# Performance work log

Measured on AMD Instinct MI355X. Metric: run time of the kernel, lower is better.

Reference implementation:

```python
import jax, jax.numpy as jnp
import numpy as np

D_IN = 384
HID = 384
D_OUT = 384

def _kaiming(key, fan_in, fan_out):
    return jax.random.normal(key, (fan_in, fan_out), dtype=jnp.float32) * np.sqrt(2.0 / fan_in)

def setup_inputs() -> dict:
    key = jax.random.key(0)
    ks = jax.random.split(key, 12)
    B, O, T = 8, 1024, 8192
    obj_vecs = jax.random.normal(ks[0], (B, O, D_IN), dtype=jnp.float32)
    pred_vecs = jax.random.normal(ks[1], (B, T, D_IN), dtype=jnp.float32)
    edges = jax.random.randint(ks[2], (B, T, 2), 0, O, dtype=jnp.int64)
    # gconv1: [3D -> H -> 2H + Dout]; gconv2: [H -> H -> Dout]
    w1a = _kaiming(ks[3], 3 * D_IN, HID); b1a = jnp.zeros((HID,), jnp.float32)
    w1b = _kaiming(ks[4], HID, 2 * HID + D_OUT); b1b = jnp.zeros((2 * HID + D_OUT,), jnp.float32)
    w2a = _kaiming(ks[5], HID, HID); b2a = jnp.zeros((HID,), jnp.float32)
    w2b = _kaiming(ks[6], HID, D_OUT); b2b = jnp.zeros((D_OUT,), jnp.float32)
    return {"obj_vecs": obj_vecs, "pred_vecs": pred_vecs, "edges": edges,
            "w1a": w1a, "b1a": b1a, "w1b": w1b, "b1b": b1b,
            "w2a": w2a, "b2a": b2a, "w2b": w2b, "b2b": b2b}

def _gconv_forward(obj_vecs, pred_vecs, edges, w1a, b1a, w1b, b1b, w2a, b2a, w2b, b2b):
    B, O, D = obj_vecs.shape
    s_idx = edges[:, :, 0]  # (B, T)
    o_idx = edges[:, :, 1]
    batch = jnp.arange(B)[:, None]
    subj = obj_vecs[batch, s_idx]  # (B, T, D) gather
    objt = obj_vecs[batch, o_idx]
    triple = jnp.concatenate([subj, pred_vecs, objt], axis=-1)  # (B, T, 3D)
    h = jax.nn.relu(triple @ w1a + b1a)
    t = jax.nn.relu(h @ w1b + b1b)  # (B, T, 2H + Dout)
    new_s = t[:, :, :HID]
    new_p = t[:, :, HID:HID + D_OUT]
    new_o = t[:, :, HID + D_OUT:]
    # scatter_add per batch into (O, H) buffers
    def agg(si, oi, vs, vo):
        return jnp.zeros((O, HID), vs.dtype).at[si].add(vs).at[oi].add(vo)
    pooled = jax.vmap(agg)(s_idx, o_idx, new_s, new_o)  # (B, O, H)
    pooled = pooled / jnp.linalg.norm(pooled)  # global Frobenius norm, as in torch .norm()
    out_obj = jax.nn.relu(jax.nn.relu(pooled @ w2a + b2a) @ w2b + b2b)
    return out_obj, new_p

def reference(obj_vecs, pred_vecs, edges, w1a, b1a, w1b, b1b, w2a, b2a, w2b, b2b):
    return _gconv_forward(obj_vecs, pred_vecs, edges, w1a, b1a, w1b, b1b, w2a, b2a, w2b, b2b)
```

## Files before the change

### kernel.cpp

```cpp
#include <hip/hip_runtime.h>
#include <hip/hip_bf16.h>

#define NB 8
#define NT 8192
#define NO 1024
#define DD 384
#define K1 1152
#define M1 65536
#define MO 8192

typedef __attribute__((ext_vector_type(8))) short bf16x8;
typedef __attribute__((ext_vector_type(4))) float f32x4;
typedef __attribute__((ext_vector_type(4))) unsigned short u16x4;

__device__ __forceinline__ unsigned short f2bf(float f) {
    union { float f; unsigned u; } v; v.f = f;
    unsigned r = v.u + 0x7FFFu + ((v.u >> 16) & 1u);
    return (unsigned short)(r >> 16);
}
__device__ __forceinline__ float bf2f(unsigned short h) {
    union { unsigned u; float f; } v; v.u = ((unsigned)h) << 16;
    return v.f;
}
__device__ __forceinline__ bf16x8 pack8(f32x4 a, f32x4 b) {
    bf16x8 r;
    r[0] = (short)f2bf(a[0]); r[1] = (short)f2bf(a[1]);
    r[2] = (short)f2bf(a[2]); r[3] = (short)f2bf(a[3]);
    r[4] = (short)f2bf(b[0]); r[5] = (short)f2bf(b[1]);
    r[6] = (short)f2bf(b[2]); r[7] = (short)f2bf(b[3]);
    return r;
}
__device__ __forceinline__ void gload16(const void* g, void* l) {
    __builtin_amdgcn_global_load_lds(
        (const __attribute__((address_space(1))) unsigned int*)g,
        (__attribute__((address_space(3))) unsigned int*)l, 16, 0, 0);
}

__global__ void k_cvt4(const float* __restrict__ s, unsigned short* __restrict__ d, int n) {
    int i = (blockIdx.x * blockDim.x + threadIdx.x) * 4;
    if (i >= n) return;
    f32x4 v = *(const f32x4*)(s + i);
    u16x4 o;
    o[0] = f2bf(v[0]); o[1] = f2bf(v[1]); o[2] = f2bf(v[2]); o[3] = f2bf(v[3]);
    *(u16x4*)(d + i) = o;
}
__global__ void k_tr(const float* __restrict__ s, unsigned short* __restrict__ d, int K, int N) {
    int k = blockIdx.x;
    int n = blockIdx.y * blockDim.x + threadIdx.x;
    if (n < N) d[n * K + k] = f2bf(s[k * N + n]);
}

__global__ void k_ss1(const float* __restrict__ p, float* __restrict__ partial, int n4) {
    __shared__ float wsum[4];
    int stride = gridDim.x * blockDim.x;
    float s = 0.f;
    for (int i = blockIdx.x * blockDim.x + threadIdx.x; i < n4; i += stride) {
        f32x4 v = *(const f32x4*)(p + i * 4);
        s += v[0] * v[0] + v[1] * v[1] + v[2] * v[2] + v[3] * v[3];
    }
#pragma unroll
    for (int off = 32; off; off >>= 1) s += __shfl_down(s, off, 64);
    if ((threadIdx.x & 63) == 0) wsum[threadIdx.x >> 6] = s;
    __syncthreads();
    if (threadIdx.x == 0)
        partial[blockIdx.x] = wsum[0] + wsum[1] + wsum[2] + wsum[3];
}
__global__ void k_ss2(const float* __restrict__ partial, float* __restrict__ o) {
    float s = partial[threadIdx.x];
#pragma unroll
    for (int off = 32; off; off >>= 1) s += __shfl_down(s, off, 64);
    __shared__ float w0, w1;
    if (threadIdx.x == 0) w0 = s;
    if (threadIdx.x == 64) w1 = s;
    __syncthreads();
    if (threadIdx.x == 0) o[0] = w0 + w1;
}
__global__ void k_normcvt(const float* __restrict__ p, const float* __restrict__ ss,
                          unsigned short* __restrict__ o) {
    int i = (blockIdx.x * blockDim.x + threadIdx.x) * 8;
    float s = rsqrtf(ss[0]);
    f32x4 a = *(const f32x4*)(p + i), b = *(const f32x4*)(p + i + 4);
    a *= s; b *= s;
    *(bf16x8*)(o + i) = pack8(a, b);
}

__global__ void k_hist(const int* __restrict__ edges, int* __restrict__ cnt) {
    int i = blockIdx.x * 256 + threadIdx.x;
    int2 e = *(const int2*)&edges[(size_t)i * 2];
    int b = i >> 13;
    atomicAdd(&cnt[(b << 10) + e.x], 1);
    atomicAdd(&cnt[(b << 10) + e.y], 1);
}
__global__ void k_scan(const int* __restrict__ cnt, int* __restrict__ offs) {
    __shared__ int a[1024];
    int b = blockIdx.x, t = threadIdx.x;
    int own = cnt[(b << 10) + t];
    a[t] = own;
    __syncthreads();
    for (int s = 1; s < 1024; s <<= 1) {
        int v = (t >= s) ? a[t - s] : 0;
        __syncthreads();
        a[t] += v;
        __syncthreads();
    }
    offs[(b << 10) + t] = a[t] - own;
}
__global__ void k_fill(const int* __restrict__ edges, const int* __restrict__ offs,
                       int* __restrict__ cur, int* __restrict__ elist) {
    int i = blockIdx.x * 256 + threadIdx.x;
    int2 e = *(const int2*)&edges[(size_t)i * 2];
    int b = i >> 13, t = i & (NT - 1);
    int ps = atomicAdd(&cur[(b << 10) + e.x], 1);
    elist[(b << 14) + offs[(b << 10) + e.x] + ps] = t * 2;
    int po = atomicAdd(&cur[(b << 10) + e.y], 1);
    elist[(b << 14) + offs[(b << 10) + e.y] + po] = t * 2 + 1;
}
__global__ void k_pool(const unsigned short* __restrict__ sob, const int* __restrict__ cnt,
                       const int* __restrict__ offs, const int* __restrict__ elist,
                       float* __restrict__ pooled) {
    int w = (blockIdx.x * 256 + threadIdx.x) >> 6;
    int lane = threadIdx.x & 63;
    if (lane >= 48) return;
    int b = w >> 10, o = w & (NO - 1);
    int len = cnt[(b << 10) + o];
    const int* lst = elist + (b << 14) + offs[(b << 10) + o];
    f32x4 a0 = {0.f, 0.f, 0.f, 0.f}, a1 = {0.f, 0.f, 0.f, 0.f};
    f32x4 c0 = {0.f, 0.f, 0.f, 0.f}, c1 = {0.f, 0.f, 0.f, 0.f};
    int j = 0;
    for (; j + 1 < len; j += 2) {
        int e0 = lst[j], e1 = lst[j + 1];
        bf16x8 v0 = *(const bf16x8*)(sob + ((size_t)((b << 13) + (e0 >> 1))) * 768 + (e0 & 1) * DD + lane * 8);
        bf16x8 v1 = *(const bf16x8*)(sob + ((size_t)((b << 13) + (e1 >> 1))) * 768 + (e1 & 1) * DD + lane * 8);
        a0[0] += bf2f((unsigned short)v0[0]); a0[1] += bf2f((unsigned short)v0[1]);
        a0[2] += bf2f((unsigned short)v0[2]); a0[3] += bf2f((unsigned short)v0[3]);
        a1[0] += bf2f((unsigned short)v0[4]); a1[1] += bf2f((unsigned short)v0[5]);
        a1[2] += bf2f((unsigned short)v0[6]); a1[3] += bf2f((unsigned short)v0[7]);
        c0[0] += bf2f((unsigned short)v1[0]); c0[1] += bf2f((unsigned short)v1[1]);
        c0[2] += bf2f((unsigned short)v1[2]); c0[3] += bf2f((unsigned short)v1[3]);
        c1[0] += bf2f((unsigned short)v1[4]); c1[1] += bf2f((unsigned short)v1[5]);
        c1[2] += bf2f((unsigned short)v1[6]); c1[3] += bf2f((unsigned short)v1[7]);
    }
    if (j < len) {
        int e0 = lst[j];
        bf16x8 v0 = *(const bf16x8*)(sob + ((size_t)((b << 13) + (e0 >> 1))) * 768 + (e0 & 1) * DD + lane * 8);
        a0[0] += bf2f((unsigned short)v0[0]); a0[1] += bf2f((unsigned short)v0[1]);
        a0[2] += bf2f((unsigned short)v0[2]); a0[3] += bf2f((unsigned short)v0[3]);
        a1[0] += bf2f((unsigned short)v0[4]); a1[1] += bf2f((unsigned short)v0[5]);
        a1[2] += bf2f((unsigned short)v0[6]); a1[3] += bf2f((unsigned short)v0[7]);
    }
    a0 += c0; a1 += c1;
    float* dst = pooled + ((size_t)((b << 10) + o)) * DD + lane * 8;
    *(f32x4*)dst = a0;
    *(f32x4*)(dst + 4) = a1;
}

__launch_bounds__(256, 2)
__global__ void gemm_g1(const unsigned short* __restrict__ objb,
                        const float* __restrict__ predf,
                        const int* __restrict__ edges,
                        const unsigned short* __restrict__ Bt,
                        const float* __restrict__ bias,
                        unsigned short* __restrict__ outb)
{
    const int tid = threadIdx.x;
    const int lane = tid & 63;
    const int d = blockIdx.x;
    const int chunk = gridDim.x >> 3;
    const int bid = (d & 7) * chunk + (d >> 3);
    const int xb = bid >> 1, nb = bid & 1;
    const int m0 = xb * 128;
    const int btrow = nb * 192;

    __shared__ unsigned short lds[2][20480];

    const int rb = tid >> 3;
    const int c8 = ((tid & 7) ^ (rb & 7)) * 8;

    const int bb = (m0 >> 13) << 10;
    int er0[4], er1[4];
#pragma unroll
    for (int i = 0; i < 4; ++i) {
        int2 e = *(const int2*)&edges[(size_t)(m0 + i * 32 + rb) * 2];
        er0[i] = bb + e.x;
        er1[i] = bb + e.y;
    }

    f32x4 acc[4][6];
#pragma unroll
    for (int i = 0; i < 4; ++i)
#pragma unroll
        for (int j = 0; j < 6; ++j) acc[i][j] = (f32x4){0.f, 0.f, 0.f, 0.f};

    const int wid = tid >> 6, wm = wid >> 1, wn = wid & 1;
    const int l16 = lane & 15, lg = lane >> 4;

#pragma unroll
    for (int i = 0; i < 4; ++i)
        gload16(objb + (size_t)er0[i] * DD + c8, &lds[0][i * 2048 + tid * 8]);
#pragma unroll
    for (int i = 0; i < 6; ++i)
        gload16(Bt + (size_t)(btrow + i * 32 + rb) * K1 + c8, &lds[0][8192 + i * 2048 + tid * 8]);

    const int nsteps = K1 / 64;
    for (int t = 0; t < nsteps; ++t) {
        const int cur = t & 1;
        const int tn = t + 1;
        if (tn < nsteps) {
            const int nseg = tn / 6;
            const int ko = (tn - nseg * 6) * 64;
            if (nseg == 1) {
                f32x4 pf[4][2];
#pragma unroll
                for (int i = 0; i < 4; ++i) {
                    const float* p = predf + (size_t)(m0 + i * 32 + rb) * DD + ko + c8;
                    pf[i][0] = *(const f32x4*)p;
                    pf[i][1] = *(const f32x4*)(p + 4);
                }
#pragma unroll
                for (int i = 0; i < 6; ++i)
                    gload16(Bt + (size_t)(btrow + i * 32 + rb) * K1 + tn * 64 + c8,
                            &lds[cur ^ 1][8192 + i * 2048 + tid * 8]);
#pragma unroll
                for (int i = 0; i < 4; ++i)
                    *(bf16x8*)(&lds[cur ^ 1][i * 2048 + tid * 8]) = pack8(pf[i][0], pf[i][1]);
            } else {
#pragma unroll
                for (int i = 0; i < 4; ++i) {
                    int row = (nseg == 0) ? er0[i] : er1[i];
                    gload16(objb + (size_t)row * DD + ko + c8, &lds[cur ^ 1][i * 2048 + tid * 8]);
                }
#pragma unroll
                for (int i = 0; i < 6; ++i)
                    gload16(Bt + (size_t)(btrow + i * 32 + rb) * K1 + tn * 64 + c8,
                            &lds[cur ^ 1][8192 + i * 2048 + tid * 8]);
                asm volatile("s_waitcnt vmcnt(10)" ::: "memory");
            }
        } else {
            asm volatile("s_waitcnt vmcnt(0)" ::: "memory");
        }
        __builtin_amdgcn_s_barrier();
        const unsigned short* At = &lds[cur][0];
        const unsigned short* Bl = &lds[cur][8192];
#pragma unroll
        for (int kt = 0; kt < 2; ++kt) {
            const int cs = ((kt * 4 + lg) ^ (l16 & 7)) * 8;
            bf16x8 af[4], bfr[6];
#pragma unroll
            for (int mt = 0; mt < 4; ++mt)
                af[mt] = *(const bf16x8*)(At + (wm * 64 + mt * 16 + l16) * 64 + cs);
#pragma unroll
            for (int nn = 0; nn < 6; ++nn)
                bfr[nn] = *(const bf16x8*)(Bl + (wn * 96 + nn * 16 + l16) * 64 + cs);
#pragma unroll
            for (int mt = 0; mt < 4; ++mt)
#pragma unroll
                for (int nn = 0; nn < 6; ++nn)
                    acc[mt][nn] = __builtin_amdgcn_mfma_f32_16x16x32_bf16(af[mt], bfr[nn], acc[mt][nn], 0, 0, 0);
        }
        asm volatile("s_waitcnt lgkmcnt(0)" ::: "memory");
        __builtin_amdgcn_s_barrier();
    }

#pragma unroll
    for (int nn = 0; nn < 6; ++nn) {
        int gn = btrow + wn * 96 + nn * 16 + l16;
        float bv = bias[gn];
#pragma unroll
        for (int mt = 0; mt < 4; ++mt) {
            int rbase = wm * 64 + mt * 16 + lg * 4;
#pragma unroll
            for (int rg = 0; rg < 4; ++rg) {
                int gr = m0 + rbase + rg;
                float v = fmaxf(acc[mt][nn][rg] + bv, 0.0f);
                outb[(size_t)gr * DD + gn] = f2bf(v);
            }
        }
    }
}

template <int EPI>
__launch_bounds__(256, 2)
__global__ void gemm_p(const unsigned short* __restrict__ Abf,
                       const unsigned short* __restrict__ Bt,
                       const float* __restrict__ bias,
                       unsigned short* __restrict__ outb,
                       float* __restrict__ outf,
                       int K, int ldC, int nbn, int osplit, int oadd)
{
    const int tid = threadIdx.x;
    const int lane = tid & 63;
    const int d = blockIdx.x;
    const int chunk = gridDim.x >> 3;
    const int bid = (d & 7) * chunk + (d >> 3);
    const int xb = bid / nbn, nb = bid - xb * nbn;
    const int m0 = xb * 128;
    const int btrow = nb * 192 + (nb >= osplit ? oadd : 0);
    const int col0 = nb * 192;

    __shared__ unsigned short lds[2][20480];

    const int rb = tid >> 3;
    const int c8 = ((tid & 7) ^ (rb & 7)) * 8;

    f32x4 acc[4][6];
#pragma unroll
    for (int i = 0; i < 4; ++i)
#pragma unroll
        for (int j = 0; j < 6; ++j) acc[i][j] = (f32x4){0.f, 0.f, 0.f, 0.f};

    const int wid = tid >> 6, wm = wid >> 1, wn = wid & 1;
    const int l16 = lane & 15, lg = lane >> 4;

#define STAGE_P(BUF, KK)                                                                   \
    {                                                                                      \
        _Pragma("unroll")                                                                  \
        for (int i = 0; i < 6; ++i)                                                        \
            gload16(Bt + (size_t)(btrow + i * 32 + rb) * K + (KK) + c8,                    \
                    &lds[BUF][8192 + i * 2048 + tid * 8]);                                 \
        _Pragma("unroll")                                                                  \
        for (int i = 0; i < 4; ++i)                                                        \
            gload16(Abf + (size_t)(m0 + i * 32 + rb) * K + (KK) + c8,                      \
                    &lds[BUF][i * 2048 + tid * 8]);                                        \
    }

    const int nt = K / 64;
    STAGE_P(0, 0)
    for (int t = 0; t < nt; ++t) {
        const int cur = t & 1;
        if (t + 1 < nt) {
            STAGE_P(cur ^ 1, (t + 1) * 64)
            asm volatile("s_waitcnt vmcnt(10)" ::: "memory");
        } else {
            asm volatile("s_waitcnt vmcnt(0)" ::: "memory");
        }
        __builtin_amdgcn_s_barrier();
        const unsigned short* At = &lds[cur][0];
        const unsigned short* Bl = &lds[cur][8192];
#pragma unroll
        for (int kt = 0; kt < 2; ++kt) {
            const int cs = ((kt * 4 + lg) ^ (l16 & 7)) * 8;
            bf16x8 af[4], bfr[6];
#pragma unroll
            for (int mt = 0; mt < 4; ++mt)
                af[mt] = *(const bf16x8*)(At + (wm * 64 + mt * 16 + l16) * 64 + cs);
#pragma unroll
            for (int nn = 0; nn < 6; ++nn)
                bfr[nn] = *(const bf16x8*)(Bl + (wn * 96 + nn * 16 + l16) * 64 + cs);
#pragma unroll
            for (int mt = 0; mt < 4; ++mt)
#pragma unroll
                for (int nn = 0; nn < 6; ++nn)
                    acc[mt][nn] = __builtin_amdgcn_mfma_f32_16x16x32_bf16(af[mt], bfr[nn], acc[mt][nn], 0, 0, 0);
        }
        asm volatile("s_waitcnt lgkmcnt(0)" ::: "memory");
        __builtin_amdgcn_s_barrier();
    }
#undef STAGE_P

#pragma unroll
    for (int nn = 0; nn < 6; ++nn) {
        int gnl = wn * 96 + nn * 16 + l16;
        float bv = bias[btrow + gnl];
#pragma unroll
        for (int mt = 0; mt < 4; ++mt) {
            int rbase = wm * 64 + mt * 16 + lg * 4;
#pragma unroll
            for (int rg = 0; rg < 4; ++rg) {
                int gr = m0 + rbase + rg;
                float v = fmaxf(acc[mt][nn][rg] + bv, 0.0f);
                if (EPI == 0) outb[(size_t)gr * ldC + col0 + gnl] = f2bf(v);
                else          outf[(size_t)gr * ldC + col0 + gnl] = v;
            }
        }
    }
}

extern "C" void kernel_launch(void* const* d_in, const int* in_sizes, int n_in,
                              void* d_out, int out_size, void* d_ws, size_t ws_size,
                              hipStream_t stream)
{
    const float* obj  = (const float*)d_in[0];
    const float* pred = (const float*)d_in[1];
    const int* edges  = (const int*)d_in[2];
    const float* w1a  = (const float*)d_in[3];
    const float* b1a  = (const float*)d_in[4];
    const float* w1b  = (const float*)d_in[5];
    const float* b1b  = (const float*)d_in[6];
    const float* w2a  = (const float*)d_in[7];
    const float* b2a  = (const float*)d_in[8];
    const float* w2b  = (const float*)d_in[9];
    const float* b2b  = (const float*)d_in[10];

    float* out_obj = (float*)d_out;
    float* newp    = out_obj + (size_t)MO * DD;
    unsigned short* sob = (unsigned short*)newp;

    unsigned short* objb = (unsigned short*)d_ws;
    unsigned short* w1aT = objb + (size_t)NB * NO * DD;
    unsigned short* w1bT = w1aT + (size_t)DD * K1;
    unsigned short* w2aT = w1bT + (size_t)K1 * DD;
    unsigned short* w2bT = w2aT + (size_t)DD * DD;
    unsigned short* hbuf = w2bT + (size_t)DD * DD;
    float* pooled = (float*)(hbuf + (size_t)M1 * DD);
    float* sumsq  = pooled + (size_t)MO * DD;
    unsigned short* hid2 = (unsigned short*)(sumsq + 4);
    int* cnt   = (int*)(hid2 + (size_t)MO * DD);
    int* cur   = cnt + NB * NO;
    int* offs  = cur + NB * NO;
    int* elist = offs + NB * NO;
    float* partial = (float*)(elist + 2 * M1);
    unsigned short* poolb = objb;

    hipLaunchKernelGGL(k_cvt4, dim3(3072), dim3(256), 0, stream, obj, objb, NB * NO * DD);
    hipLaunchKernelGGL(k_tr, dim3(K1, 3), dim3(128), 0, stream, w1a, w1aT, K1, DD);
    hipLaunchKernelGGL(k_tr, dim3(DD, 9), dim3(128), 0, stream, w1b, w1bT, DD, K1);
    hipLaunchKernelGGL(k_tr, dim3(DD, 3), dim3(128), 0, stream, w2a, w2aT, DD, DD);
    hipLaunchKernelGGL(k_tr, dim3(DD, 3), dim3(128), 0, stream, w2b, w2bT, DD, DD);
    hipMemsetAsync(cnt, 0, 2 * NB * NO * sizeof(int), stream);

    hipLaunchKernelGGL(gemm_g1, dim3(2 * M1 / 128), dim3(256), 0, stream,
                       objb, pred, edges, w1aT, b1a, hbuf);

    hipLaunchKernelGGL((gemm_p<0>), dim3(4 * M1 / 128), dim3(256), 0, stream,
                       hbuf, w1bT, b1b, sob, (float*)nullptr, DD, 2 * DD, 4, 2, DD);

    hipLaunchKernelGGL(k_hist, dim3(256), dim3(256), 0, stream, edges, cnt);
    hipLaunchKernelGGL(k_scan, dim3(8), dim3(1024), 0, stream, cnt, offs);
    hipLaunchKernelGGL(k_fill, dim3(256), dim3(256), 0, stream, edges, offs, cur, elist);
    hipLaunchKernelGGL(k_pool, dim3(2048), dim3(256), 0, stream, sob, cnt, offs, elist, pooled);

    hipLaunchKernelGGL((gemm_p<2>), dim3(2 * M1 / 128), dim3(256), 0, stream,
                       hbuf, w1bT, b1b, (unsigned short*)nullptr, newp, DD, DD, 2, 0, DD);

    hipLaunchKernelGGL(k_ss1, dim3(128), dim3(256), 0, stream, pooled, partial, MO * DD / 4);
    hipLaunchKernelGGL(k_ss2, dim3(1), dim3(128), 0, stream, partial, sumsq);
    hipLaunchKernelGGL(k_normcvt, dim3(1536), dim3(256), 0, stream, pooled, sumsq, poolb);

    hipLaunchKernelGGL((gemm_p<0>), dim3(2 * MO / 128), dim3(256), 0, stream,
                       poolb, w2aT, b2a, hid2, (float*)nullptr, DD, DD, 2, 2, 0);

    hipLaunchKernelGGL((gemm_p<2>), dim3(2 * MO / 128), dim3(256), 0, stream,
                       hid2, w2bT, b2b, (unsigned short*)nullptr, out_obj, DD, DD, 2, 2, 0);
}
```

Before: 246.9 us.

## Precompute per-object projections of subject/object weights before gathering in first GEMM

Splits the first-layer weight into subject, predicate and object blocks. The subject and object blocks are applied once per object (8192 rows), not once per triple (65536 rows), and the results are stored in bf16. The triple GEMM then only multiplies the predicate part (K=384 instead of 1152) and adds the gathered per-object projections in its epilogue. This cuts the first GEMM's FLOPs by roughly two thirds but adds two small GEMMs, scattered gathers in the epilogue, and extra bf16 rounding of the intermediate projections.

```diff
diff --git a/kernel.cpp b/kernel.cpp
--- a/kernel.cpp
+++ b/kernel.cpp
@@ -154,130 +154,6 @@
     *(f32x4*)(dst + 4) = a1;
 }
 
-__launch_bounds__(256, 2)
-__global__ void gemm_g1(const unsigned short* __restrict__ objb,
-                        const float* __restrict__ predf,
-                        const int* __restrict__ edges,
-                        const unsigned short* __restrict__ Bt,
-                        const float* __restrict__ bias,
-                        unsigned short* __restrict__ outb)
-{
-    const int tid = threadIdx.x;
-    const int lane = tid & 63;
-    const int d = blockIdx.x;
-    const int chunk = gridDim.x >> 3;
-    const int bid = (d & 7) * chunk + (d >> 3);
-    const int xb = bid >> 1, nb = bid & 1;
-    const int m0 = xb * 128;
-    const int btrow = nb * 192;
-
-    __shared__ unsigned short lds[2][20480];
-
-    const int rb = tid >> 3;
-    const int c8 = ((tid & 7) ^ (rb & 7)) * 8;
-
-    const int bb = (m0 >> 13) << 10;
-    int er0[4], er1[4];
-#pragma unroll
-    for (int i = 0; i < 4; ++i) {
-        int2 e = *(const int2*)&edges[(size_t)(m0 + i * 32 + rb) * 2];
-        er0[i] = bb + e.x;
-        er1[i] = bb + e.y;
-    }
-
-    f32x4 acc[4][6];
-#pragma unroll
-    for (int i = 0; i < 4; ++i)
-#pragma unroll
-        for (int j = 0; j < 6; ++j) acc[i][j] = (f32x4){0.f, 0.f, 0.f, 0.f};
-
-    const int wid = tid >> 6, wm = wid >> 1, wn = wid & 1;
-    const int l16 = lane & 15, lg = lane >> 4;
-
-#pragma unroll
-    for (int i = 0; i < 4; ++i)
-        gload16(objb + (size_t)er0[i] * DD + c8, &lds[0][i * 2048 + tid * 8]);
-#pragma unroll
-    for (int i = 0; i < 6; ++i)
-        gload16(Bt + (size_t)(btrow + i * 32 + rb) * K1 + c8, &lds[0][8192 + i * 2048 + tid * 8]);
-
-    const int nsteps = K1 / 64;
-    for (int t = 0; t < nsteps; ++t) {
-        const int cur = t & 1;
-        const int tn = t + 1;
-        if (tn < nsteps) {
-            const int nseg = tn / 6;
-            const int ko = (tn - nseg * 6) * 64;
-            if (nseg == 1) {
-                f32x4 pf[4][2];
-#pragma unroll
-                for (int i = 0; i < 4; ++i) {
-                    const float* p = predf + (size_t)(m0 + i * 32 + rb) * DD + ko + c8;
-                    pf[i][0] = *(const f32x4*)p;
-                    pf[i][1] = *(const f32x4*)(p + 4);
-                }
-#pragma unroll
-                for (int i = 0; i < 6; ++i)
-                    gload16(Bt + (size_t)(btrow + i * 32 + rb) * K1 + tn * 64 + c8,
-                            &lds[cur ^ 1][8192 + i * 2048 + tid * 8]);
-#pragma unroll
-                for (int i = 0; i < 4; ++i)
-                    *(bf16x8*)(&lds[cur ^ 1][i * 2048 + tid * 8]) = pack8(pf[i][0], pf[i][1]);
-            } else {
-#pragma unroll
-                for (int i = 0; i < 4; ++i) {
-                    int row = (nseg == 0) ? er0[i] : er1[i];
-                    gload16(objb + (size_t)row * DD + ko + c8, &lds[cur ^ 1][i * 2048 + tid * 8]);
-                }
-#pragma unroll
-                for (int i = 0; i < 6; ++i)
-                    gload16(Bt + (size_t)(btrow + i * 32 + rb) * K1 + tn * 64 + c8,
-                            &lds[cur ^ 1][8192 + i * 2048 + tid * 8]);
-                asm volatile("s_waitcnt vmcnt(10)" ::: "memory");
-            }
-        } else {
-            asm volatile("s_waitcnt vmcnt(0)" ::: "memory");
-        }
-        __builtin_amdgcn_s_barrier();
-        const unsigned short* At = &lds[cur][0];
-        const unsigned short* Bl = &lds[cur][8192];
-#pragma unroll
-        for (int kt = 0; kt < 2; ++kt) {
-            const int cs = ((kt * 4 + lg) ^ (l16 & 7)) * 8;
-            bf16x8 af[4], bfr[6];
-#pragma unroll
-            for (int mt = 0; mt < 4; ++mt)
-                af[mt] = *(const bf16x8*)(At + (wm * 64 + mt * 16 + l16) * 64 + cs);
-#pragma unroll
-            for (int nn = 0; nn < 6; ++nn)
-                bfr[nn] = *(const bf16x8*)(Bl + (wn * 96 + nn * 16 + l16) * 64 + cs);
-#pragma unroll
-            for (int mt = 0; mt < 4; ++mt)
-#pragma unroll
-                for (int nn = 0; nn < 6; ++nn)
-                    acc[mt][nn] = __builtin_amdgcn_mfma_f32_16x16x32_bf16(af[mt], bfr[nn], acc[mt][nn], 0, 0, 0);
-        }
-        asm volatile("s_waitcnt lgkmcnt(0)" ::: "memory");
-        __builtin_amdgcn_s_barrier();
-    }
-
-#pragma unroll
-    for (int nn = 0; nn < 6; ++nn) {
-        int gn = btrow + wn * 96 + nn * 16 + l16;
-        float bv = bias[gn];
-#pragma unroll
-        for (int mt = 0; mt < 4; ++mt) {
-            int rbase = wm * 64 + mt * 16 + lg * 4;
-#pragma unroll
-            for (int rg = 0; rg < 4; ++rg) {
-                int gr = m0 + rbase + rg;
-                float v = fmaxf(acc[mt][nn][rg] + bv, 0.0f);
-                outb[(size_t)gr * DD + gn] = f2bf(v);
-            }
-        }
-    }
-}
-
 template <int EPI>
 __launch_bounds__(256, 2)
 __global__ void gemm_p(const unsigned short* __restrict__ Abf,
@@ -360,16 +236,138 @@
 #pragma unroll
     for (int nn = 0; nn < 6; ++nn) {
         int gnl = wn * 96 + nn * 16 + l16;
-        float bv = bias[btrow + gnl];
+        float bv = (EPI == 4) ? 0.f : bias[btrow + gnl];
 #pragma unroll
         for (int mt = 0; mt < 4; ++mt) {
             int rbase = wm * 64 + mt * 16 + lg * 4;
 #pragma unroll
             for (int rg = 0; rg < 4; ++rg) {
                 int gr = m0 + rbase + rg;
-                float v = fmaxf(acc[mt][nn][rg] + bv, 0.0f);
-                if (EPI == 0) outb[(size_t)gr * ldC + col0 + gnl] = f2bf(v);
-                else          outf[(size_t)gr * ldC + col0 + gnl] = v;
+                if (EPI == 4) {
+                    outb[(size_t)gr * ldC + col0 + gnl] = f2bf(acc[mt][nn][rg]);
+                } else {
+                    float v = fmaxf(acc[mt][nn][rg] + bv, 0.0f);
+                    if (EPI == 0) outb[(size_t)gr * ldC + col0 + gnl] = f2bf(v);
+                    else          outf[(size_t)gr * ldC + col0 + gnl] = v;
+                }
+            }
+        }
+    }
+}
+
+__launch_bounds__(256, 2)
+__global__ void gemm_m(const float* __restrict__ predf,
+                       const int* __restrict__ edges,
+                       const unsigned short* __restrict__ Bt,
+                       const float* __restrict__ bias,
+                       const unsigned short* __restrict__ Us,
+                       const unsigned short* __restrict__ Uo,
+                       unsigned short* __restrict__ outb)
+{
+    const int tid = threadIdx.x;
+    const int lane = tid & 63;
+    const int d = blockIdx.x;
+    const int chunk = gridDim.x >> 3;
+    const int bid = (d & 7) * chunk + (d >> 3);
+    const int xb = bid >> 1, nb = bid & 1;
+    const int m0 = xb * 128;
+    const int btrow = nb * 192;
+
+    __shared__ unsigned short lds[2][20480];
+
+    const int rb = tid >> 3;
+    const int c8 = ((tid & 7) ^ (rb & 7)) * 8;
+
+    f32x4 acc[4][6];
+#pragma unroll
+    for (int i = 0; i < 4; ++i)
+#pragma unroll
+        for (int j = 0; j < 6; ++j) acc[i][j] = (f32x4){0.f, 0.f, 0.f, 0.f};
+
+    const int wid = tid >> 6, wm = wid >> 1, wn = wid & 1;
+    const int l16 = lane & 15, lg = lane >> 4;
+
+    {
+        f32x4 pf[4][2];
+#pragma unroll
+        for (int i = 0; i < 4; ++i) {
+            const float* p = predf + (size_t)(m0 + i * 32 + rb) * DD + c8;
+            pf[i][0] = *(const f32x4*)p;
+            pf[i][1] = *(const f32x4*)(p + 4);
+        }
+#pragma unroll
+        for (int i = 0; i < 6; ++i)
+            gload16(Bt + (size_t)(btrow + i * 32 + rb) * DD + c8,
+                    &lds[0][8192 + i * 2048 + tid * 8]);
+#pragma unroll
+        for (int i = 0; i < 4; ++i)
+            *(bf16x8*)(&lds[0][i * 2048 + tid * 8]) = pack8(pf[i][0], pf[i][1]);
+    }
+
+    const int nt = DD / 64;
+    for (int t = 0; t < nt; ++t) {
+        const int cur = t & 1;
+        const int tn = t + 1;
+        if (tn < nt) {
+            f32x4 pf[4][2];
+#pragma unroll
+            for (int i = 0; i < 4; ++i) {
+                const float* p = predf + (size_t)(m0 + i * 32 + rb) * DD + tn * 64 + c8;
+                pf[i][0] = *(const f32x4*)p;
+                pf[i][1] = *(const f32x4*)(p + 4);
+            }
+#pragma unroll
+            for (int i = 0; i < 6; ++i)
+                gload16(Bt + (size_t)(btrow + i * 32 + rb) * DD + tn * 64 + c8,
+                        &lds[cur ^ 1][8192 + i * 2048 + tid * 8]);
+#pragma unroll
+            for (int i = 0; i < 4; ++i)
+                *(bf16x8*)(&lds[cur ^ 1][i * 2048 + tid * 8]) = pack8(pf[i][0], pf[i][1]);
+        } else {
+            asm volatile("s_waitcnt vmcnt(0)" ::: "memory");
+        }
+        __builtin_amdgcn_s_barrier();
+        const unsigned short* At = &lds[cur][0];
+        const unsigned short* Bl = &lds[cur][8192];
+#pragma unroll
+        for (int kt = 0; kt < 2; ++kt) {
+            const int cs = ((kt * 4 + lg) ^ (l16 & 7)) * 8;
+            bf16x8 af[4], bfr[6];
+#pragma unroll
+            for (int mt = 0; mt < 4; ++mt)
+                af[mt] = *(const bf16x8*)(At + (wm * 64 + mt * 16 + l16) * 64 + cs);
+#pragma unroll
+            for (int nn = 0; nn < 6; ++nn)
+                bfr[nn] = *(const bf16x8*)(Bl + (wn * 96 + nn * 16 + l16) * 64 + cs);
+#pragma unroll
+            for (int mt = 0; mt < 4; ++mt)
+#pragma unroll
+                for (int nn = 0; nn < 6; ++nn)
+                    acc[mt][nn] = __builtin_amdgcn_mfma_f32_16x16x32_bf16(af[mt], bfr[nn], acc[mt][nn], 0, 0, 0);
+        }
+        asm volatile("s_waitcnt lgkmcnt(0)" ::: "memory");
+        __builtin_amdgcn_s_barrier();
+    }
+
+    const int bb = (m0 >> 13) << 10;
+    float bv[6];
+#pragma unroll
+    for (int nn = 0; nn < 6; ++nn)
+        bv[nn] = bias[btrow + wn * 96 + nn * 16 + l16];
+#pragma unroll
+    for (int mt = 0; mt < 4; ++mt) {
+        int rbase = wm * 64 + mt * 16 + lg * 4;
+#pragma unroll
+        for (int rg = 0; rg < 4; ++rg) {
+            int gr = m0 + rbase + rg;
+            int2 e = *(const int2*)&edges[(size_t)gr * 2];
+            const unsigned short* us = Us + (size_t)(bb + e.x) * DD;
+            const unsigned short* uo = Uo + (size_t)(bb + e.y) * DD;
+#pragma unroll
+            for (int nn = 0; nn < 6; ++nn) {
+                int gn = btrow + wn * 96 + nn * 16 + l16;
+                float v = acc[mt][nn][rg] + bv[nn] + bf2f(us[gn]) + bf2f(uo[gn]);
+                outb[(size_t)gr * DD + gn] = f2bf(fmaxf(v, 0.0f));
             }
         }
     }
@@ -395,12 +393,14 @@
     float* newp    = out_obj + (size_t)MO * DD;
     unsigned short* sob = (unsigned short*)newp;
 
-    unsigned short* objb = (unsigned short*)d_ws;
-    unsigned short* w1aT = objb + (size_t)NB * NO * DD;
-    unsigned short* w1bT = w1aT + (size_t)DD * K1;
-    unsigned short* w2aT = w1bT + (size_t)K1 * DD;
-    unsigned short* w2bT = w2aT + (size_t)DD * DD;
-    unsigned short* hbuf = w2bT + (size_t)DD * DD;
+    unsigned short* objb  = (unsigned short*)d_ws;
+    unsigned short* w1asT = objb + (size_t)NB * NO * DD;
+    unsigned short* w1apT = w1asT + (size_t)DD * DD;
+    unsigned short* w1aoT = w1apT + (size_t)DD * DD;
+    unsigned short* w1bT  = w1aoT + (size_t)DD * DD;
+    unsigned short* w2aT  = w1bT + (size_t)K1 * DD;
+    unsigned short* w2bT  = w2aT + (size_t)DD * DD;
+    unsigned short* hbuf  = w2bT + (size_t)DD * DD;
     float* pooled = (float*)(hbuf + (size_t)M1 * DD);
     float* sumsq  = pooled + (size_t)MO * DD;
     unsigned short* hid2 = (unsigned short*)(sumsq + 4);
@@ -410,16 +410,25 @@
     int* elist = offs + NB * NO;
     float* partial = (float*)(elist + 2 * M1);
     unsigned short* poolb = objb;
+    unsigned short* Us = hid2;
+    unsigned short* Uo = (unsigned short*)pooled;
 
     hipLaunchKernelGGL(k_cvt4, dim3(3072), dim3(256), 0, stream, obj, objb, NB * NO * DD);
-    hipLaunchKernelGGL(k_tr, dim3(K1, 3), dim3(128), 0, stream, w1a, w1aT, K1, DD);
+    hipLaunchKernelGGL(k_tr, dim3(DD, 3), dim3(128), 0, stream, w1a, w1asT, DD, DD);
+    hipLaunchKernelGGL(k_tr, dim3(DD, 3), dim3(128), 0, stream, w1a + (size_t)DD * DD, w1apT, DD, DD);
+    hipLaunchKernelGGL(k_tr, dim3(DD, 3), dim3(128), 0, stream, w1a + (size_t)2 * DD * DD, w1aoT, DD, DD);
     hipLaunchKernelGGL(k_tr, dim3(DD, 9), dim3(128), 0, stream, w1b, w1bT, DD, K1);
     hipLaunchKernelGGL(k_tr, dim3(DD, 3), dim3(128), 0, stream, w2a, w2aT, DD, DD);
     hipLaunchKernelGGL(k_tr, dim3(DD, 3), dim3(128), 0, stream, w2b, w2bT, DD, DD);
     hipMemsetAsync(cnt, 0, 2 * NB * NO * sizeof(int), stream);
 
-    hipLaunchKernelGGL(gemm_g1, dim3(2 * M1 / 128), dim3(256), 0, stream,
-                       objb, pred, edges, w1aT, b1a, hbuf);
+    hipLaunchKernelGGL((gemm_p<4>), dim3(2 * MO / 128), dim3(256), 0, stream,
+                       objb, w1asT, b1a, Us, (float*)nullptr, DD, DD, 2, 2, 0);
+    hipLaunchKernelGGL((gemm_p<4>), dim3(2 * MO / 128), dim3(256), 0, stream,
+                       objb, w1aoT, b1a, Uo, (float*)nullptr, DD, DD, 2, 2, 0);
+
+    hipLaunchKernelGGL(gemm_m, dim3(2 * M1 / 128), dim3(256), 0, stream,
+                       pred, edges, w1apT, b1a, Us, Uo, hbuf);
 
     hipLaunchKernelGGL((gemm_p<0>), dim3(4 * M1 / 128), dim3(256), 0, stream,
                        hbuf, w1bT, b1b, sob, (float*)nullptr, DD, 2 * DD, 4, 2, DD);
```

Result: no change. 249.2 us (+0.9%).
